# Optimization experiments

Hardware: AMD Instinct MI355X
Metric: run time of the kernel (lower is better)

The kernel has to match this reference:

```python
import jax, jax.numpy as jnp
import numpy as np
from jax import lax

N = 2                      # half phase-space dim (q1,q2 / p1,p2)
NUM_MACRO_STEPS = 32
TOT_SECS = 1.0
DIM = N + N**2 + N**3 + N**4 + N**5   # 62 monomials up to degree 5
BATCH = 65536


def _features(x):
    """x: [b, 2] -> [b, 62] monomials of degree 1..5 (with repeats, as in torch code)."""
    b = x.shape[0]
    quad = (x[:, :, None] * x[:, None, :]).reshape(b, N**2)
    cub = (quad[:, :, None] * x[:, None, :]).reshape(b, N**3)
    quart = (cub[:, :, None] * x[:, None, :]).reshape(b, N**4)
    quint = (quart[:, :, None] * x[:, None, :]).reshape(b, N**5)
    return jnp.concatenate([x, quad, cub, quart, quint], axis=1)


def _poly_grad(x, w):
    """grad wrt x of sum_b features(x) @ w  ->  [b, 2] (samples independent)."""
    return jax.grad(lambda xx: jnp.sum(_features(xx) @ w))(x)


def _flow(z, A_w, B_w, C_w, D_w, dt):
    def step(z, ws):
        aw, bw, cw, dw = ws
        q, p = z[:, 0:2], z[:, 2:4]
        # A half-step (dA_p computed once and reused, matching the torch code)
        dA = _poly_grad(p, aw)
        q = q + dA * (0.5 * dt)
        # B full step
        dB = _poly_grad(q, bw)
        p = p - dB * dt
        # second A half-step with the ORIGINAL dA (faithful to source)
        q = q + dA * (0.5 * dt)
        # z = [q1, q2, p1, p2]; u = (q2, p1), v = (q1, p2)
        u = jnp.concatenate([q[:, 1:2], p[:, 0:1]], axis=1)
        v = jnp.concatenate([q[:, 0:1], p[:, 1:2]], axis=1)
        # C half-step on u using rotated grad of C(v)
        dC = _poly_grad(v, cw)
        dCmod = jnp.concatenate([dC[:, 1:2], -dC[:, 0:1]], axis=1)
        u = u + dCmod * (0.5 * dt)
        # D full step on v using rotated grad of D(u)
        dD = _poly_grad(u, dw)
        dDmod = jnp.concatenate([dD[:, 1:2], -dD[:, 0:1]], axis=1)
        v = v + dDmod * dt
        # second C half-step with the ORIGINAL dCmod (faithful to source)
        u = u + dCmod * (0.5 * dt)
        z = jnp.concatenate([v[:, 0:1], u, v[:, 1:2]], axis=1)
        return z, None

    z, _ = lax.scan(step, z, (A_w, B_w, C_w, D_w))
    return z


def setup_inputs() -> dict:
    key = jax.random.key(0)
    kz, ka, kb, kc, kd = jax.random.split(key, 5)
    return {
        "z_init": jax.random.normal(kz, (BATCH, 4), dtype=jnp.float32),
        "A_w": 0.02 * jax.random.normal(ka, (NUM_MACRO_STEPS, DIM), dtype=jnp.float32),
        "B_w": 0.02 * jax.random.normal(kb, (NUM_MACRO_STEPS, DIM), dtype=jnp.float32),
        "C_w": 0.02 * jax.random.normal(kc, (NUM_MACRO_STEPS, DIM), dtype=jnp.float32),
        "D_w": 0.02 * jax.random.normal(kd, (NUM_MACRO_STEPS, DIM), dtype=jnp.float32),
        "num_steps": 10,
    }


def reference(z_init, A_w, B_w, C_w, D_w, num_steps):
    dt = TOT_SECS / (NUM_MACRO_STEPS * float(num_steps))
    return _flow(z_init, A_w, B_w, C_w, D_w, dt)
```

## Files before the change

kernel.cpp:

```cpp
#include <hip/hip_runtime.h>
#include <stdint.h>

#define NSTEP 32

typedef _Float16 h2 __attribute__((ext_vector_type(2)));

__device__ __forceinline__ h2 toh2(uint32_t w) { return __builtin_bit_cast(h2, w); }

__device__ __forceinline__ void loadstep(const uint32_t* __restrict__ sg, uint32_t (&R)[60]) {
#pragma unroll
    for (int i = 0; i < 15; ++i) {
        uint4 v = *reinterpret_cast<const uint4*>(sg + i * 4);
        R[i * 4 + 0] = v.x; R[i * 4 + 1] = v.y;
        R[i * 4 + 2] = v.z; R[i * 4 + 3] = v.w;
    }
}

template <int B>
__device__ __forceinline__ void pgrad(const uint32_t (&g)[60], h2 xm, h2 xo,
                                      float& d0, float& d1) {
    h2 r0 = toh2(g[B + 4]);
    r0 = r0 * xm + toh2(g[B + 3]);
    r0 = r0 * xm + toh2(g[B + 2]);
    r0 = r0 * xm + toh2(g[B + 1]);
    r0 = r0 * xm + toh2(g[B + 0]);
    h2 r1 = toh2(g[B + 8]);
    r1 = r1 * xm + toh2(g[B + 7]);
    r1 = r1 * xm + toh2(g[B + 6]);
    r1 = r1 * xm + toh2(g[B + 5]);
    h2 r2 = toh2(g[B + 11]);
    r2 = r2 * xm + toh2(g[B + 10]);
    r2 = r2 * xm + toh2(g[B + 9]);
    h2 r3 = toh2(g[B + 13]);
    r3 = r3 * xm + toh2(g[B + 12]);
    h2 acc = toh2(g[B + 14]);
    acc = acc * xo + r3;
    acc = acc * xo + r2;
    acc = acc * xo + r1;
    acc = acc * xo + r0;
    d0 = (float)acc.x;
    d1 = (float)acc.y;
}

__device__ __forceinline__ void mkpair(float x0, float x1, h2& xm, h2& xo) {
    xo = __builtin_bit_cast(h2, __builtin_amdgcn_cvt_pkrtz(x0, x1));
    xm = __builtin_bit_cast(h2, __builtin_amdgcn_cvt_pkrtz(x1, x0));
}

__device__ __forceinline__ void dostep(const uint32_t (&g)[60], float& q0, float& q1,
                                       float& p0, float& p1, float dt, float hdt) {
    h2 xm, xo;

    mkpair(p0, p1, xm, xo);
    float dA0, dA1; pgrad<0>(g, xm, xo, dA0, dA1);
    q0 = fmaf(dA0, hdt, q0); q1 = fmaf(dA1, hdt, q1);

    mkpair(q0, q1, xm, xo);
    float dB0, dB1; pgrad<15>(g, xm, xo, dB0, dB1);
    p0 = fmaf(-dB0, dt, p0); p1 = fmaf(-dB1, dt, p1);
    q0 = fmaf(dA0, hdt, q0); q1 = fmaf(dA1, hdt, q1);

    float u0 = q1, u1 = p0, v0 = q0, v1 = p1;

    mkpair(v0, v1, xm, xo);
    float dC0, dC1; pgrad<30>(g, xm, xo, dC0, dC1);
    u0 = fmaf(dC1, hdt, u0); u1 = fmaf(-dC0, hdt, u1);

    mkpair(u0, u1, xm, xo);
    float dD0, dD1; pgrad<45>(g, xm, xo, dD0, dD1);
    v0 = fmaf(dD1, dt, v0); v1 = fmaf(-dD0, dt, v1);
    u0 = fmaf(dC1, hdt, u0); u1 = fmaf(-dC0, hdt, u1);

    q0 = v0; q1 = u0; p0 = u1; p1 = v1;
}

__global__ void __launch_bounds__(256, 1)
sympl_fused(const float* __restrict__ zin,
            const float* __restrict__ Aw, const float* __restrict__ Bw,
            const float* __restrict__ Cw, const float* __restrict__ Dw,
            const int* __restrict__ nsp,
            float* __restrict__ zout, int batch) {
    __shared__ uint32_t sGp[NSTEP * 64];

    int lt = threadIdx.x;
    int idx = blockIdx.x * 256 + lt;
    bool active = idx < batch;

    float4 zv = make_float4(0.f, 0.f, 0.f, 0.f);
    if (active) zv = reinterpret_cast<const float4*>(zin)[idx];
    float dt  = 1.0f / (32.0f * (float)nsp[0]);
    float hdt = 0.5f * dt;

    if (lt < NSTEP * 4) {
        int stepi = lt >> 2, which = lt & 3;
        const float* w;
        switch (which) { case 0: w = Aw; break; case 1: w = Bw; break;
                         case 2: w = Cw; break; default: w = Dw; }
        w += stepi * 62;
        const float2* w2 = reinterpret_cast<const float2*>(w);

        float c[6][6];
#pragma unroll
        for (int a = 0; a < 6; ++a)
#pragma unroll
            for (int b = 0; b < 6; ++b) c[a][b] = 0.f;
#pragma unroll
        for (int d = 1; d <= 5; ++d) {
            int base2 = ((1 << d) - 2) >> 1;
#pragma unroll
            for (int fp = 0; fp < (1 << d) / 2; ++fp) {
                float2 v = w2[base2 + fp];
                int b = __popc(2 * fp);
                c[d - b][b]         += v.x;
                c[d - b - 1][b + 1] += v.y;
            }
        }

        float g0[15], g1[15];
        int k = 0;
#pragma unroll
        for (int e0 = 0; e0 <= 4; ++e0)
#pragma unroll
            for (int e1 = 0; e1 + e0 <= 4; ++e1)
                g0[k++] = (float)(e0 + 1) * c[e0 + 1][e1];
        k = 0;
#pragma unroll
        for (int e1 = 0; e1 <= 4; ++e1)
#pragma unroll
            for (int e0 = 0; e0 + e1 <= 4; ++e0)
                g1[k++] = (float)(e1 + 1) * c[e0][e1 + 1];

        uint32_t* dst = sGp + stepi * 64 + which * 15;
#pragma unroll
        for (int i = 0; i < 15; ++i) {
            h2 h; h.x = (_Float16)g0[i]; h.y = (_Float16)g1[i];
            dst[i] = __builtin_bit_cast(uint32_t, h);
        }
        if (which == 0) { sGp[stepi * 64 + 60] = 0u; sGp[stepi * 64 + 61] = 0u;
                          sGp[stepi * 64 + 62] = 0u; sGp[stepi * 64 + 63] = 0u; }
    }
    __syncthreads();

    float q0 = zv.x, q1 = zv.y, p0 = zv.z, p1 = zv.w;

    uint32_t bufX[60], bufY[60];
    loadstep(sGp, bufX);

#pragma unroll 1
    for (int it = 0; it < NSTEP / 2; ++it) {
        int s = 2 * it;
        loadstep(sGp + (s + 1) * 64, bufY);
        dostep(bufX, q0, q1, p0, p1, dt, hdt);
        int sn = (s + 2 < NSTEP) ? s + 2 : NSTEP - 1;
        loadstep(sGp + sn * 64, bufX);
        dostep(bufY, q0, q1, p0, p1, dt, hdt);
    }

    if (active) {
        float4 o; o.x = q0; o.y = q1; o.z = p0; o.w = p1;
        reinterpret_cast<float4*>(zout)[idx] = o;
    }
}

extern "C" void kernel_launch(void* const* d_in, const int* in_sizes, int n_in,
                              void* d_out, int out_size, void* d_ws, size_t ws_size,
                              hipStream_t stream) {
    const float* z  = (const float*)d_in[0];
    const float* Aw = (const float*)d_in[1];
    const float* Bw = (const float*)d_in[2];
    const float* Cw = (const float*)d_in[3];
    const float* Dw = (const float*)d_in[4];
    const int*   ns = (const int*)d_in[5];

    int batch = in_sizes[0] / 4;
    int threads = 256;
    int blocks = (batch + threads - 1) / threads;
    sympl_fused<<<blocks, threads, 0, stream>>>(z, Aw, Bw, Cw, Dw, ns,
                                                (float*)d_out, batch);
}
```

Measured before the change: 15.46 us.

## Process two samples per thread to amortize LDS coefficient loads

Halves the block to 128 threads, with each thread integrating two samples that share the same per-step coefficient registers loaded from LDS. This halves the LDS traffic per sample and gives the scheduler two independent dependency chains to interleave, hiding FMA latency. In exchange it uses more registers and launches half as many wavefronts, so fewer waves are available for latency hiding.

```diff
diff --git a/kernel.cpp b/kernel.cpp
--- a/kernel.cpp
+++ b/kernel.cpp
@@ -47,34 +47,44 @@
     xm = __builtin_bit_cast(h2, __builtin_amdgcn_cvt_pkrtz(x1, x0));
 }
 
-__device__ __forceinline__ void dostep(const uint32_t (&g)[60], float& q0, float& q1,
-                                       float& p0, float& p1, float dt, float hdt) {
+__device__ __forceinline__ void dostep2(const uint32_t (&g)[60],
+                                        float (&q0)[2], float (&q1)[2],
+                                        float (&p0)[2], float (&p1)[2],
+                                        float dt, float hdt) {
     h2 xm, xo;
-
-    mkpair(p0, p1, xm, xo);
-    float dA0, dA1; pgrad<0>(g, xm, xo, dA0, dA1);
-    q0 = fmaf(dA0, hdt, q0); q1 = fmaf(dA1, hdt, q1);
-
-    mkpair(q0, q1, xm, xo);
-    float dB0, dB1; pgrad<15>(g, xm, xo, dB0, dB1);
-    p0 = fmaf(-dB0, dt, p0); p1 = fmaf(-dB1, dt, p1);
-    q0 = fmaf(dA0, hdt, q0); q1 = fmaf(dA1, hdt, q1);
-
-    float u0 = q1, u1 = p0, v0 = q0, v1 = p1;
-
-    mkpair(v0, v1, xm, xo);
-    float dC0, dC1; pgrad<30>(g, xm, xo, dC0, dC1);
-    u0 = fmaf(dC1, hdt, u0); u1 = fmaf(-dC0, hdt, u1);
-
-    mkpair(u0, u1, xm, xo);
-    float dD0, dD1; pgrad<45>(g, xm, xo, dD0, dD1);
-    v0 = fmaf(dD1, dt, v0); v1 = fmaf(-dD0, dt, v1);
-    u0 = fmaf(dC1, hdt, u0); u1 = fmaf(-dC0, hdt, u1);
-
-    q0 = v0; q1 = u0; p0 = u1; p1 = v1;
+    float dA0[2], dA1[2];
+#pragma unroll
+    for (int j = 0; j < 2; ++j) {
+        mkpair(p0[j], p1[j], xm, xo);
+        pgrad<0>(g, xm, xo, dA0[j], dA1[j]);
+        q0[j] = fmaf(dA0[j], hdt, q0[j]); q1[j] = fmaf(dA1[j], hdt, q1[j]);
+    }
+#pragma unroll
+    for (int j = 0; j < 2; ++j) {
+        mkpair(q0[j], q1[j], xm, xo);
+        float dB0, dB1; pgrad<15>(g, xm, xo, dB0, dB1);
+        p0[j] = fmaf(-dB0, dt, p0[j]); p1[j] = fmaf(-dB1, dt, p1[j]);
+        q0[j] = fmaf(dA0[j], hdt, q0[j]); q1[j] = fmaf(dA1[j], hdt, q1[j]);
+    }
+    float u0[2], u1[2], v0[2], v1[2], dC0[2], dC1[2];
+#pragma unroll
+    for (int j = 0; j < 2; ++j) {
+        u0[j] = q1[j]; u1[j] = p0[j]; v0[j] = q0[j]; v1[j] = p1[j];
+        mkpair(v0[j], v1[j], xm, xo);
+        pgrad<30>(g, xm, xo, dC0[j], dC1[j]);
+        u0[j] = fmaf(dC1[j], hdt, u0[j]); u1[j] = fmaf(-dC0[j], hdt, u1[j]);
+    }
+#pragma unroll
+    for (int j = 0; j < 2; ++j) {
+        mkpair(u0[j], u1[j], xm, xo);
+        float dD0, dD1; pgrad<45>(g, xm, xo, dD0, dD1);
+        v0[j] = fmaf(dD1, dt, v0[j]); v1[j] = fmaf(-dD0, dt, v1[j]);
+        u0[j] = fmaf(dC1[j], hdt, u0[j]); u1[j] = fmaf(-dC0[j], hdt, u1[j]);
+        q0[j] = v0[j]; q1[j] = u0[j]; p0[j] = u1[j]; p1[j] = v1[j];
+    }
 }
 
-__global__ void __launch_bounds__(256, 1)
+__global__ void __launch_bounds__(128, 1)
 sympl_fused(const float* __restrict__ zin,
             const float* __restrict__ Aw, const float* __restrict__ Bw,
             const float* __restrict__ Cw, const float* __restrict__ Dw,
@@ -83,15 +93,18 @@
     __shared__ uint32_t sGp[NSTEP * 64];
 
     int lt = threadIdx.x;
-    int idx = blockIdx.x * 256 + lt;
-    bool active = idx < batch;
+    int base = blockIdx.x * 256;
+    int i0 = base + lt, i1 = base + 128 + lt;
+    bool a0 = i0 < batch, a1 = i1 < batch;
 
-    float4 zv = make_float4(0.f, 0.f, 0.f, 0.f);
-    if (active) zv = reinterpret_cast<const float4*>(zin)[idx];
+    float4 zv0 = make_float4(0.f, 0.f, 0.f, 0.f);
+    float4 zv1 = make_float4(0.f, 0.f, 0.f, 0.f);
+    if (a0) zv0 = reinterpret_cast<const float4*>(zin)[i0];
+    if (a1) zv1 = reinterpret_cast<const float4*>(zin)[i1];
     float dt  = 1.0f / (32.0f * (float)nsp[0]);
     float hdt = 0.5f * dt;
 
-    if (lt < NSTEP * 4) {
+    {
         int stepi = lt >> 2, which = lt & 3;
         const float* w;
         switch (which) { case 0: w = Aw; break; case 1: w = Bw; break;
@@ -141,7 +154,8 @@
     }
     __syncthreads();
 
-    float q0 = zv.x, q1 = zv.y, p0 = zv.z, p1 = zv.w;
+    float q0[2] = {zv0.x, zv1.x}, q1[2] = {zv0.y, zv1.y};
+    float p0[2] = {zv0.z, zv1.z}, p1[2] = {zv0.w, zv1.w};
 
     uint32_t bufX[60], bufY[60];
     loadstep(sGp, bufX);
@@ -150,15 +164,19 @@
     for (int it = 0; it < NSTEP / 2; ++it) {
         int s = 2 * it;
         loadstep(sGp + (s + 1) * 64, bufY);
-        dostep(bufX, q0, q1, p0, p1, dt, hdt);
+        dostep2(bufX, q0, q1, p0, p1, dt, hdt);
         int sn = (s + 2 < NSTEP) ? s + 2 : NSTEP - 1;
         loadstep(sGp + sn * 64, bufX);
-        dostep(bufY, q0, q1, p0, p1, dt, hdt);
+        dostep2(bufY, q0, q1, p0, p1, dt, hdt);
     }
 
-    if (active) {
-        float4 o; o.x = q0; o.y = q1; o.z = p0; o.w = p1;
-        reinterpret_cast<float4*>(zout)[idx] = o;
+    if (a0) {
+        float4 o; o.x = q0[0]; o.y = q1[0]; o.z = p0[0]; o.w = p1[0];
+        reinterpret_cast<float4*>(zout)[i0] = o;
+    }
+    if (a1) {
+        float4 o; o.x = q0[1]; o.y = q1[1]; o.z = p0[1]; o.w = p1[1];
+        reinterpret_cast<float4*>(zout)[i1] = o;
     }
 }
 
@@ -173,8 +191,7 @@
     const int*   ns = (const int*)d_in[5];
 
     int batch = in_sizes[0] / 4;
-    int threads = 256;
-    int blocks = (batch + threads - 1) / threads;
-    sympl_fused<<<blocks, threads, 0, stream>>>(z, Aw, Bw, Cw, Dw, ns,
-                                                (float*)d_out, batch);
+    int blocks = (batch + 255) / 256;
+    sympl_fused<<<blocks, 128, 0, stream>>>(z, Aw, Bw, Cw, Dw, ns,
+                                            (float*)d_out, batch);
 }
```

Result: slower. 19.49 us, median of 2 (+26.1%).
